# Kernel tuning notes

Hardware: AMD Instinct MI355X
Metric: run time of the kernel (lower is better)

## Reference

```python
import jax, jax.numpy as jnp
import numpy as np

C = 256
A = 3
N = 2
LV = [(160, 240, 4), (80, 120, 8), (40, 60, 16), (20, 30, 32), (10, 15, 64)]  # (H, W, stride)
LVTOP = 1000
IOU_THR = 0.7
POST_TOP = 1000


def _make_priors(h, w, stride):
    ys = (np.arange(h) + 0.5) * stride
    xs = (np.arange(w) + 0.5) * stride
    cy, cx = np.meshgrid(ys, xs, indexing='ij')
    ratios = np.array([0.5, 1.0, 2.0])
    size = stride * 4.0
    ws = size * np.sqrt(ratios)
    hs = size / np.sqrt(ratios)
    x1 = cx[..., None] - ws / 2
    y1 = cy[..., None] - hs / 2
    x2 = cx[..., None] + ws / 2
    y2 = cy[..., None] + hs / 2
    return np.stack([x1, y1, x2, y2], -1).reshape(-1, 4).astype(np.float32)


def setup_inputs() -> dict:
    key = jax.random.key(0)
    ks = jax.random.split(key, 9)
    inp = {}
    for i, (h, w, s) in enumerate(LV):
        inp[f'fmap{i}'] = jax.random.normal(ks[i], (N, C, h, w), jnp.float32)
        inp[f'priors{i}'] = jnp.asarray(_make_priors(h, w, s))
    inp['imsizes'] = jnp.array([[640.0, 960.0]] * N, jnp.float32)  # (h, w) per image
    inp['conv_w'] = jax.random.normal(ks[5], (C, C, 3, 3), jnp.float32) * 0.02
    inp['conv_b'] = jnp.zeros((C,), jnp.float32)
    inp['log_w'] = jax.random.normal(ks[6], (A, C), jnp.float32) * 0.02
    inp['log_b'] = jnp.zeros((A,), jnp.float32)
    inp['reg_w'] = jax.random.normal(ks[7], (A * 4, C), jnp.float32) * 0.02
    inp['reg_b'] = jnp.zeros((A * 4,), jnp.float32)
    return inp


def _forward(fmaps, priors, imsizes, conv_w, conv_b, log_w, log_b, reg_w, reg_b):
    n = fmaps[0].shape[0]
    boxes_l, logit_l, lvidx_l = [], [], []
    for lv, (x, p) in enumerate(zip(fmaps, priors)):
        # 3x3 conv head + relu
        h = jax.lax.conv_general_dilated(x, conv_w, (1, 1), [(1, 1), (1, 1)],
                                         dimension_numbers=('NCHW', 'OIHW', 'NCHW'))
        h = jax.nn.relu(h + conv_b[None, :, None, None])
        # 1x1 heads, permute(0,2,3,1).reshape  -> [n, H*W*A, 4] / [n, H*W*A]
        reg = jnp.einsum('nchw,oc->nhwo', h, reg_w) + reg_b
        log = jnp.einsum('nchw,oc->nhwo', h, log_w) + log_b
        reg = jax.lax.stop_gradient(reg.reshape(n, -1, 4))  # .detach() in torch
        log = jax.lax.stop_gradient(log.reshape(n, -1))
        k = min(LVTOP, log.shape[1])
        val, top = jax.lax.top_k(log, k)                    # per-image level-wise topk
        regt = jnp.take_along_axis(reg, top[..., None], axis=1)  # [n,k,4]
        prit = p[top]                                       # [n,k,4]
        # decode_boxes with mults (1, 1): priors xyxy -> cxcywh, apply deltas
        pw = prit[..., 2] - prit[..., 0]
        ph = prit[..., 3] - prit[..., 1]
        pcx = prit[..., 0] + 0.5 * pw
        pcy = prit[..., 1] + 0.5 * ph
        cx = pcx + regt[..., 0] * pw
        cy = pcy + regt[..., 1] * ph
        bw = pw * jnp.exp(regt[..., 2])
        bh = ph * jnp.exp(regt[..., 3])
        boxes_l.append(jnp.stack([cx - bw / 2, cy - bh / 2, cx + bw / 2, cy + bh / 2], -1))
        logit_l.append(val)
        lvidx_l.append(jnp.full((k,), lv, jnp.int32))
    boxes = jnp.concatenate(boxes_l, 1)                     # [n, K, 4]
    obj = jax.nn.sigmoid(jnp.concatenate(logit_l, 1))       # [n, K]
    lvidx = jnp.concatenate(lvidx_l)                        # [K]
    K = boxes.shape[1]
    # flatten; obj >= 0 keeps everything (sigmoid), min_size=0 removes nothing
    boxes = boxes.reshape(-1, 4)
    obj = obj.reshape(-1)
    imidx = jnp.repeat(jnp.arange(n), K)
    lvidx = jnp.tile(lvidx, n)
    # clamp_to_canvas
    hw = imsizes[imidx]                                     # [M, 2] = (h, w)
    xs = jnp.clip(boxes[:, 0::2], 0.0, hw[:, 1:2])
    ys = jnp.clip(boxes[:, 1::2], 0.0, hw[:, 0:1])
    boxes = jnp.stack([xs[:, 0], ys[:, 0], xs[:, 1], ys[:, 1]], -1)
    # batched_nms via coordinate-offset trick; groups = imidx*10 + level
    groups = (imidx * 10 + lvidx).astype(boxes.dtype)
    off = groups * (jnp.max(boxes) + 1.0)
    bo = boxes + off[:, None]
    order = jnp.argsort(-obj)
    bs = bo[order]
    ss = obj[order]
    ims = imidx[order]
    braw = boxes[order]
    M = bs.shape[0]
    area = (bs[:, 2] - bs[:, 0]) * (bs[:, 3] - bs[:, 1])
    rng = jnp.arange(M)

    def body(i, keep):
        cur = bs[i]
        ix1 = jnp.maximum(cur[0], bs[:, 0])
        iy1 = jnp.maximum(cur[1], bs[:, 1])
        ix2 = jnp.minimum(cur[2], bs[:, 2])
        iy2 = jnp.minimum(cur[3], bs[:, 3])
        inter = jnp.clip(ix2 - ix1, 0.0) * jnp.clip(iy2 - iy1, 0.0)
        iou = inter / jnp.maximum(area[i] + area - inter, 1e-9)
        sup = (iou > IOU_THR) & (rng > i) & keep[i]
        return keep & ~sup

    keep = jax.lax.fori_loop(0, M, body, jnp.ones((M,), bool))
    # per-image top POST_TOP kept boxes, in score order (fixed-shape padded output)
    outs_b, outs_i = [], []
    for i in range(n):
        m = keep & (ims == i)
        sc = jnp.where(m, ss, -jnp.inf)
        v, idx = jax.lax.top_k(sc, POST_TOP)
        valid = v > -jnp.inf
        outs_b.append(jnp.where(valid[:, None], braw[idx], 0.0))
        outs_i.append(jnp.where(valid, i, -1))
    return jnp.stack(outs_b), jnp.stack(outs_i)


def reference(fmap0, fmap1, fmap2, fmap3, fmap4,
              priors0, priors1, priors2, priors3, priors4,
              imsizes, conv_w, conv_b, log_w, log_b, reg_w, reg_b):
    fmaps = [fmap0, fmap1, fmap2, fmap3, fmap4]
    priors = [priors0, priors1, priors2, priors3, priors4]
    return _forward(fmaps, priors, imsizes, conv_w, conv_b, log_w, log_b, reg_w, reg_b)
```

## Files before the change

### kernel.cpp

```cpp
#include <hip/hip_runtime.h>

#define TOTA 153450
#define NGRP 10
#define CK 4
#define CAND_CAP 4096
#define SENT (-3.0e38f)

__device__ __forceinline__ int lv_base(int lv) {
  switch (lv) { case 0: return 0; case 1: return 115200; case 2: return 144000;
                case 3: return 151200; default: return 153000; }
}
__device__ __forceinline__ int lv_of_anchor(int a) {
  if (a < 115200) return 0;
  if (a < 144000) return 1;
  if (a < 151200) return 2;
  if (a < 153000) return 3;
  return 4;
}
__device__ __forceinline__ int kk_of(int lv) { return lv == 4 ? 450 : 1000; }

__device__ __forceinline__ unsigned fkey32(float f) {
  unsigned u = __float_as_uint(f);
  return (u & 0x80000000u) ? ~u : (u | 0x80000000u);
}
__device__ __forceinline__ float inv_fkey32(unsigned k) {
  unsigned u = (k & 0x80000000u) ? (k & 0x7FFFFFFFu) : ~k;
  return __uint_as_float(u);
}

__device__ __forceinline__ float cr_expf(float x) { return (float)exp((double)x); }
__device__ __forceinline__ float cr_sigmoidf(float x) {
  float t = (float)exp(-(double)x);
  float d = 1.0f + t;
  return 1.0f / d;
}

__global__ void transpose_w_kernel(const float* __restrict__ CW, float* __restrict__ WT) {
  int i = blockIdx.x*256 + threadIdx.x;
  if (i >= 2304*256) return;
  int co = i / 2304;
  int k  = i - co*2304;
  WT[(size_t)k*256 + co] = CW[i];
}

#define PPT 2
#define SPT 32
#define XCOLS 34
__global__ __launch_bounds__(256) void conv_head_kernel(
    const float* __restrict__ WT, const float* __restrict__ CB,
    const float* __restrict__ LW, const float* __restrict__ LB,
    const float* __restrict__ RW, const float* __restrict__ RB,
    const float* __restrict__ f0, const float* __restrict__ f1,
    const float* __restrict__ f2, const float* __restrict__ f3,
    const float* __restrict__ f4,
    float* __restrict__ outLog, float* __restrict__ outReg)
{
#pragma clang fp contract(off)
  constexpr int SMEM0 = CK*9*256*4 + 3*CK*XCOLS*4;
  constexpr int SMEM = (SMEM0 > 31744) ? SMEM0 : 31744;
  __shared__ __align__(16) char smem[SMEM];
  float* WS = (float*)smem;
  float* XS = (float*)(smem + CK*9*256*4);
  const int tid = threadIdx.x;
  const int sp = tid & 15;
  const int cg = tid >> 4;

  int bx = blockIdx.x;
  int lv, local;
  if (bx < 1280)      { lv = 0; local = bx; }
  else if (bx < 1600) { lv = 1; local = bx - 1280; }
  else if (bx < 1680) { lv = 2; local = bx - 1600; }
  else if (bx < 1700) { lv = 3; local = bx - 1680; }
  else                { lv = 4; local = bx - 1700; }
  const int TXN[5] = {8, 4, 2, 1, 1};
  const int LH[5]  = {160, 80, 40, 20, 10};
  const int LW_[5] = {240, 120, 60, 30, 15};
  int tx = local % TXN[lv];
  int y  = local / TXN[lv];
  int H = LH[lv], W = LW_[lv];
  int abase = lv_base(lv);
  const float* Xb;
  switch (lv) { case 0: Xb = f0; break; case 1: Xb = f1; break; case 2: Xb = f2; break;
                case 3: Xb = f3; break; default: Xb = f4; }
  const int img = blockIdx.z;
  const float* X = Xb + (size_t)img*256*H*W;
  float* oLog = outLog + (size_t)img*TOTA;
  float* oReg = outReg + (size_t)img*TOTA*4;
  const int x0 = tx * SPT;

  float acc[PPT][16];
  float acc2[PPT][16];
#pragma unroll
  for (int p = 0; p < PPT; ++p)
#pragma unroll
    for (int i = 0; i < 16; ++i) { acc[p][i] = 0.f; acc2[p][i] = 0.f; }

  for (int c0 = 0; c0 < 256; c0 += CK) {
    __syncthreads();
    {
      const float4* wsrc = (const float4*)(WT + (size_t)c0*9*256);
      float4* wdst = (float4*)WS;
#pragma unroll
      for (int r = 0; r < 9; ++r)
        wdst[r*256 + tid] = wsrc[r*256 + tid];
    }
    for (int t = tid; t < 3*CK*XCOLS; t += 256) {
      int col = t % XCOLS; int r = t / XCOLS;
      int ci = r % CK, ry = r / CK;
      int ix = x0 + col - 1, iy = y + ry - 1;
      float v = 0.f;
      if (ix >= 0 && ix < W && iy >= 0 && iy < H)
        v = X[((c0+ci)*H + iy)*W + ix];
      XS[r*XCOLS + col] = v;
    }
    __syncthreads();
#pragma unroll
    for (int ci = 0; ci < CK; ++ci) {
      int ch9 = (c0 + ci) * 9;
#pragma unroll
      for (int k9 = 0; k9 < 9; ++k9) {
        int kglob = ch9 + k9;
        if (kglob == 384 || kglob == 768 || kglob == 1152 ||
            kglob == 1536 || kglob == 1920) {
#pragma unroll
          for (int p = 0; p < PPT; ++p)
#pragma unroll
            for (int i = 0; i < 16; ++i) { acc2[p][i] = acc2[p][i] + acc[p][i]; acc[p][i] = 0.f; }
        }
        int ky = k9 / 3, kx = k9 - ky*3;
        const float* xb = &XS[(ky*CK + ci)*XCOLS + sp + kx];
        float dxv[PPT];
#pragma unroll
        for (int p = 0; p < PPT; ++p) dxv[p] = xb[p*16];
        const float* wr = &WS[(ci*9 + k9)*256 + cg*16];
#pragma unroll
        for (int i = 0; i < 16; i += 4) {
          float4 w4 = *(const float4*)(wr + i);
#pragma unroll
          for (int p = 0; p < PPT; ++p) {
            acc[p][i+0] = fmaf(w4.x, dxv[p], acc[p][i+0]);
            acc[p][i+1] = fmaf(w4.y, dxv[p], acc[p][i+1]);
            acc[p][i+2] = fmaf(w4.z, dxv[p], acc[p][i+2]);
            acc[p][i+3] = fmaf(w4.w, dxv[p], acc[p][i+3]);
          }
        }
      }
    }
  }
  __syncthreads();
  float* HS = (float*)smem;
  float* HWT = (float*)(smem + 16384);
  for (int t = tid; t < 15*256; t += 256) {
    int o = t >> 8, c = t & 255;
    HWT[t] = (o < 3) ? LW[o*256 + c] : RW[(o-3)*256 + c];
  }
#pragma unroll
  for (int px = 0; px < PPT; ++px) {
    __syncthreads();
#pragma unroll
    for (int i = 0; i < 16; ++i) {
      float hsum = acc2[px][i] + acc[px][i];
      float v = hsum + CB[cg*16 + i];
      HS[(cg*16 + i)*16 + sp] = v > 0.f ? v : 0.f;
    }
    __syncthreads();
    if (cg < 15) {
      const float* wr = &HWT[cg*256];
      float a2 = 0.f;
      for (int c = 0; c < 256; ++c) {
        float p = HS[c*16 + sp] * wr[c];
        a2 = a2 + p;
      }
      int gx = x0 + px*16 + sp;
      if (gx < W) {
        int locg = y*W + gx;
        if (cg < 3) {
          oLog[abase + locg*3 + cg] = a2 + LB[cg];
        } else {
          int oo = cg - 3;
          oReg[(size_t)(abase + locg*3 + (oo >> 2))*4 + (oo & 3)] = a2 + RB[oo];
        }
      }
    }
  }
}

__global__ void hist_kernel(const float* __restrict__ logits, unsigned* __restrict__ hist) {
  int i = blockIdx.x*256 + threadIdx.x;
  if (i >= 2*TOTA) return;
  int img = i / TOTA, a = i - img*TOTA;
  int lv = lv_of_anchor(a);
  unsigned k = fkey32(logits[i]);
  atomicAdd(&hist[(size_t)(img*5+lv)*65536 + (k >> 16)], 1u);
}

__global__ __launch_bounds__(256) void thresh_kernel(const unsigned* __restrict__ hist,
                                                     int* __restrict__ meta) {
  int g = blockIdx.x;
  const unsigned* hg = hist + (size_t)g*65536;
  __shared__ unsigned part[256];
  int tid = threadIdx.x;
  unsigned s = 0;
  for (int b = tid*256; b < tid*256 + 256; ++b) s += hg[b];
  part[tid] = s;
  __syncthreads();
  if (tid == 0) {
    int k = kk_of(g % 5);
    unsigned cum = 0; int gsel = 0;
    for (int j = 255; j >= 0; --j) {
      if (cum + part[j] >= (unsigned)k) { gsel = j; break; }
      cum += part[j];
    }
    int B = gsel*256;
    for (int b = gsel*256 + 255; b >= gsel*256; --b) {
      unsigned h = hg[b];
      if (cum + h >= (unsigned)k) { B = b; break; }
      cum += h;
    }
    meta[g] = B;
  }
}

__global__ void collect_kernel(const float* __restrict__ logits, const int* __restrict__ meta,
                               int* __restrict__ ccnt, unsigned long long* __restrict__ cand) {
  int i = blockIdx.x*256 + threadIdx.x;
  if (i >= 2*TOTA) return;
  int img = i / TOTA, a = i - img*TOTA;
  int lv = lv_of_anchor(a);
  int g = img*5 + lv;
  unsigned k = fkey32(logits[i]);
  if ((int)(k >> 16) >= meta[g]) {
    int p = atomicAdd(&ccnt[g], 1);
    if (p < CAND_CAP) {
      unsigned idx = (unsigned)(a - lv_base(lv));
      cand[(size_t)g*CAND_CAP + p] =
          ((unsigned long long)k << 32) | (unsigned long long)(0xFFFFFFFFu ^ idx);
    }
  }
}

__global__ __launch_bounds__(1024) void selsort_kernel(
    const int* __restrict__ ccnt, const unsigned long long* __restrict__ cand,
    float* __restrict__ sellk, unsigned* __restrict__ seli, int* __restrict__ selcnt)
{
  __shared__ unsigned long long KS[CAND_CAP];
  int g = blockIdx.x, tid = threadIdx.x;
  int n = ccnt[g]; if (n > CAND_CAP) n = CAND_CAP;
  for (int t = tid; t < CAND_CAP; t += 1024)
    KS[t] = (t < n) ? cand[(size_t)g*CAND_CAP + t] : 0ULL;
  __syncthreads();
  for (int k2 = 2; k2 <= CAND_CAP; k2 <<= 1)
    for (int j = k2 >> 1; j > 0; j >>= 1) {
      for (int t = tid; t < CAND_CAP/2; t += 1024) {
        int i = (t/j)*(2*j) + (t%j);
        int ix = i + j;
        bool up = ((i & k2) == 0);
        unsigned long long a = KS[i], b = KS[ix];
        if ((a < b) == up) { KS[i] = b; KS[ix] = a; }
      }
      __syncthreads();
    }
  int k = kk_of(g % 5);
  if (tid == 0) selcnt[g] = k;
  for (int t = tid; t < 1024; t += 1024) {
    if (t < k) {
      unsigned long long e = KS[t];
      sellk[(size_t)g*1024 + t] = inv_fkey32((unsigned)(e >> 32));
      seli[(size_t)g*1024 + t] = 0xFFFFFFFFu ^ (unsigned)(e & 0xFFFFFFFFULL);
    } else {
      sellk[(size_t)g*1024 + t] = SENT;
      seli[(size_t)g*1024 + t] = 0u;
    }
  }
}

__global__ __launch_bounds__(1024) void decode_kernel(
    const unsigned* __restrict__ seli, const float* __restrict__ sellk,
    const int* __restrict__ selcnt,
    const float* __restrict__ reg, const float* __restrict__ imsz,
    const float* __restrict__ p0, const float* __restrict__ p1, const float* __restrict__ p2,
    const float* __restrict__ p3, const float* __restrict__ p4,
    float* __restrict__ boxesF, float* __restrict__ selv32)
{
#pragma clang fp contract(off)
  int g = blockIdx.x, t = threadIdx.x;
  int img = g/5, lv = g - img*5;
  int k = selcnt[g];
  float b0 = 0, b1 = 0, b2 = 0, b3 = 0;
  float sv = SENT;
  if (t < k) {
    unsigned aidx = seli[(size_t)g*1024 + t];
    const float* pr;
    switch (lv) { case 0: pr = p0; break; case 1: pr = p1; break; case 2: pr = p2; break;
                  case 3: pr = p3; break; default: pr = p4; }
    pr += (size_t)aidx*4;
    const float* rg = reg + ((size_t)img*TOTA + lv_base(lv) + aidx)*4;
    float q0 = pr[0], q1 = pr[1], q2 = pr[2], q3 = pr[3];
    float pw = q2 - q0, ph = q3 - q1;
    float pcx = q0 + 0.5f*pw, pcy = q1 + 0.5f*ph;
    float t0 = rg[0]*pw, t1 = rg[1]*ph;
    float cx = pcx + t0, cy = pcy + t1;
    float e2 = cr_expf(rg[2]);
    float e3 = cr_expf(rg[3]);
    float bw = pw*e2, bh = ph*e3;
    float x1 = cx - bw*0.5f, y1 = cy - bh*0.5f, x2 = cx + bw*0.5f, y2 = cy + bh*0.5f;
    float mh = imsz[img*2 + 0], mw = imsz[img*2 + 1];
    b0 = fminf(fmaxf(x1, 0.f), mw);
    b1 = fminf(fmaxf(y1, 0.f), mh);
    b2 = fminf(fmaxf(x2, 0.f), mw);
    b3 = fminf(fmaxf(y2, 0.f), mh);
    sv = cr_sigmoidf(sellk[(size_t)g*1024 + t]);
  }
  float* o = boxesF + ((size_t)g*1024 + t)*4;
  o[0] = b0; o[1] = b1; o[2] = b2; o[3] = b3;
  selv32[(size_t)g*1024 + t] = sv;
}

__global__ void maxbox_kernel(const float* __restrict__ boxesF, unsigned* __restrict__ maxbuf) {
  int i = blockIdx.x*1024 + threadIdx.x;
  if (i < NGRP*1024*4) {
    float v = boxesF[i];
    atomicMax(maxbuf, __float_as_uint(v));
  }
}

__global__ __launch_bounds__(256) void mask_kernel(
    const float* __restrict__ boxesF, const int* __restrict__ selcnt,
    const unsigned* __restrict__ maxbuf, unsigned long long* __restrict__ supm)
{
#pragma clang fp contract(off)
  __shared__ float4 BS[1024];
  __shared__ float AR[1024];
  int g = blockIdx.y;
  int i = blockIdx.x*16 + (threadIdx.x >> 4);
  int w = threadIdx.x & 15;
  int img = g/5, lv = g - img*5;
  int k = selcnt[g];
  float mx1 = __uint_as_float(*maxbuf) + 1.0f;
  float offv = (float)(img*10 + lv) * mx1;
  for (int t = threadIdx.x; t < 1024; t += 256) {
    float4 b = ((const float4*)boxesF)[(size_t)g*1024 + t];
    b.x = b.x + offv; b.y = b.y + offv; b.z = b.z + offv; b.w = b.w + offv;
    BS[t] = b;
    float dw = b.z - b.x, dh = b.w - b.y;
    AR[t] = dw*dh;
  }
  __syncthreads();
  unsigned long long m = 0ULL;
  if (i < k) {
    float4 bi = BS[i]; float ai = AR[i];
    int jbase = w*64;
    for (int jj = 0; jj < 64; ++jj) {
      int j = jbase + jj;
      if (j > i && j < k) {
        float4 bj = BS[j];
        float ix1 = fmaxf(bi.x, bj.x), iy1 = fmaxf(bi.y, bj.y);
        float ix2 = fminf(bi.z, bj.z), iy2 = fminf(bi.w, bj.w);
        float d1 = fmaxf(ix2 - ix1, 0.f), d2 = fmaxf(iy2 - iy1, 0.f);
        float inter = d1*d2;
        float un = ai + AR[j];
        un = un - inter;
        float iou = inter / fmaxf(un, 1e-9f);
        if (iou > 0.7f) m |= (1ULL << jj);
      }
    }
  }
  supm[((size_t)g*1024 + i)*16 + w] = m;
}

__global__ __launch_bounds__(64) void nms_scan_kernel(
    const unsigned long long* __restrict__ supm, const int* __restrict__ selcnt,
    unsigned long long* __restrict__ keepw)
{
  __shared__ unsigned long long rem[16];
  int g = blockIdx.x, l = threadIdx.x;
  if (l < 16) rem[l] = 0ULL;
  __syncthreads();
  int k = selcnt[g];
  for (int i = 0; i < k; ++i) {
    bool sup = (rem[i >> 6] >> (i & 63)) & 1ULL;
    __syncthreads();
    if (!sup && l < 16) rem[l] |= supm[((size_t)g*1024 + i)*16 + l];
    __syncthreads();
  }
  if (l < 16) keepw[g*16 + l] = ~rem[l];
}

__global__ __launch_bounds__(1024) void final_kernel(
    const float* __restrict__ selv32, const int* __restrict__ selcnt,
    const unsigned long long* __restrict__ keepw, const float* __restrict__ boxesF,
    float* __restrict__ outB, float* __restrict__ outI)
{
  extern __shared__ unsigned long long S[];
  int img = blockIdx.x, tid = threadIdx.x;
  for (int t = tid; t < 8192; t += 1024) {
    unsigned long long key = 0ULL;
    if (t < 5000) {
      int lv = t / 1000, r = t - lv*1000;
      int g = img*5 + lv;
      if (r < selcnt[g] && ((keepw[g*16 + (r >> 6)] >> (r & 63)) & 1ULL)) {
        float sv = selv32[(size_t)g*1024 + r];
        key = ((unsigned long long)fkey32(sv) << 32) |
              (unsigned long long)(0xFFFFFFFFu ^ (unsigned)t);
      }
    }
    S[t] = key;
  }
  __syncthreads();
  for (int k2 = 2; k2 <= 8192; k2 <<= 1)
    for (int j = k2 >> 1; j > 0; j >>= 1) {
      for (int t = tid; t < 4096; t += 1024) {
        int i = (t/j)*(2*j) + (t%j);
        int ix = i + j;
        bool up = ((i & k2) == 0);
        unsigned long long a = S[i], b = S[ix];
        if ((a < b) == up) { S[i] = b; S[ix] = a; }
      }
      __syncthreads();
    }
  for (int t = tid; t < 1000; t += 1024) {
    unsigned long long key = S[t];
    float4 bo = make_float4(0.f, 0.f, 0.f, 0.f);
    float ii = -1.f;
    if (key != 0ULL) {
      unsigned slot = 0xFFFFFFFFu ^ (unsigned)(key & 0xFFFFFFFFULL);
      int lv = slot / 1000, r = slot - lv*1000;
      const float* bp = boxesF + (((size_t)(img*5 + lv))*1024 + r)*4;
      bo = make_float4(bp[0], bp[1], bp[2], bp[3]);
      ii = (float)img;
    }
    ((float4*)outB)[img*1000 + t] = bo;
    outI[img*1000 + t] = ii;
  }
}

extern "C" void kernel_launch(void* const* d_in, const int* in_sizes, int n_in,
                              void* d_out, int out_size, void* d_ws, size_t ws_size,
                              hipStream_t stream)
{
  const float* fm[5]; const float* pri[5];
  if (n_in >= 17 && in_sizes[1] == 460800) {
    for (int i = 0; i < 5; ++i) { fm[i] = (const float*)d_in[2*i]; pri[i] = (const float*)d_in[2*i+1]; }
  } else {
    for (int i = 0; i < 5; ++i) { fm[i] = (const float*)d_in[i]; pri[i] = (const float*)d_in[5+i]; }
  }
  const float* imsz  = (const float*)d_in[10];
  const float* convw = (const float*)d_in[11];
  const float* convb = (const float*)d_in[12];
  const float* logw  = (const float*)d_in[13];
  const float* logb  = (const float*)d_in[14];
  const float* regw  = (const float*)d_in[15];
  const float* regb  = (const float*)d_in[16];

  char* ws = (char*)d_ws;
  size_t off = 0;
  auto nxt = [&](size_t b) { size_t o = off; off = (off + b + 255) & ~(size_t)255; return o; };
  float* WT        = (float*)(ws + nxt((size_t)2304*256*4));
  float* logitsF   = (float*)(ws + nxt((size_t)2*TOTA*4));
  float* regF      = (float*)(ws + nxt((size_t)2*TOTA*4*4));
  unsigned* hist   = (unsigned*)(ws + nxt((size_t)NGRP*65536*4));
  int* meta        = (int*)(ws + nxt((size_t)NGRP*4));
  int* ccnt        = (int*)(ws + nxt((size_t)NGRP*4));
  unsigned long long* cand = (unsigned long long*)(ws + nxt((size_t)NGRP*CAND_CAP*8));
  float* sellk     = (float*)(ws + nxt((size_t)NGRP*1024*4));
  unsigned* seli   = (unsigned*)(ws + nxt((size_t)NGRP*1024*4));
  int* selcnt      = (int*)(ws + nxt((size_t)NGRP*4));
  float* selv32    = (float*)(ws + nxt((size_t)NGRP*1024*4));
  float* boxesF    = (float*)(ws + nxt((size_t)NGRP*1024*4*4));
  unsigned* maxbuf = (unsigned*)(ws + nxt(4));
  unsigned long long* supm  = (unsigned long long*)(ws + nxt((size_t)NGRP*1024*16*8));
  unsigned long long* keepw = (unsigned long long*)(ws + nxt((size_t)NGRP*16*8));
  if (off > ws_size) return;

  hipMemsetAsync(hist, 0, (size_t)NGRP*65536*4, stream);
  hipMemsetAsync(ccnt, 0, NGRP*4, stream);
  hipMemsetAsync(maxbuf, 0, 4, stream);

  transpose_w_kernel<<<2304, 256, 0, stream>>>(convw, WT);

  {
    dim3 grid(1710, 1, 2);
    conv_head_kernel<<<grid, 256, 0, stream>>>(
        WT, convb, logw, logb, regw, regb,
        fm[0], fm[1], fm[2], fm[3], fm[4],
        logitsF, regF);
  }
  int tot = 2*TOTA;
  hist_kernel<<<(tot + 255)/256, 256, 0, stream>>>(logitsF, hist);
  thresh_kernel<<<NGRP, 256, 0, stream>>>(hist, meta);
  collect_kernel<<<(tot + 255)/256, 256, 0, stream>>>(logitsF, meta, ccnt, cand);
  selsort_kernel<<<NGRP, 1024, 0, stream>>>(ccnt, cand, sellk, seli, selcnt);
  decode_kernel<<<NGRP, 1024, 0, stream>>>(seli, sellk, selcnt, regF, imsz,
      pri[0], pri[1], pri[2], pri[3], pri[4], boxesF, selv32);
  maxbox_kernel<<<(NGRP*1024*4 + 1023)/1024, 1024, 0, stream>>>(boxesF, maxbuf);
  mask_kernel<<<dim3(64, NGRP), 256, 0, stream>>>(boxesF, selcnt, maxbuf, supm);
  nms_scan_kernel<<<NGRP, 64, 0, stream>>>(supm, selcnt, keepw);
  final_kernel<<<2, 1024, 65536, stream>>>(selv32, selcnt, keepw, boxesF,
      (float*)d_out, (float*)d_out + 8000);
}
```

Before: 2.639 ms.

## Register-prefetch next conv channel chunk and use shuffles in NMS scan

```diff
diff --git a/kernel.cpp b/kernel.cpp
--- a/kernel.cpp
+++ b/kernel.cpp
@@ -46,7 +46,8 @@
 #define PPT 2
 #define SPT 32
 #define XCOLS 34
-__global__ __launch_bounds__(256) void conv_head_kernel(
+#define XSN (3*CK*XCOLS)
+__global__ __launch_bounds__(256, 4) void conv_head_kernel(
     const float* __restrict__ WT, const float* __restrict__ CB,
     const float* __restrict__ LW, const float* __restrict__ LB,
     const float* __restrict__ RW, const float* __restrict__ RB,
@@ -56,7 +57,7 @@
     float* __restrict__ outLog, float* __restrict__ outReg)
 {
 #pragma clang fp contract(off)
-  constexpr int SMEM0 = CK*9*256*4 + 3*CK*XCOLS*4;
+  constexpr int SMEM0 = CK*9*256*4 + XSN*4;
   constexpr int SMEM = (SMEM0 > 31744) ? SMEM0 : 31744;
   __shared__ __align__(16) char smem[SMEM];
   float* WS = (float*)smem;
@@ -95,25 +96,41 @@
 #pragma unroll
     for (int i = 0; i < 16; ++i) { acc[p][i] = 0.f; acc2[p][i] = 0.f; }
 
+  float4 wpre[9];
+  float xpre[2];
+  auto prefetch = [&](int c0) {
+    const float4* wsrc = (const float4*)(WT + (size_t)c0*9*256);
+#pragma unroll
+    for (int r = 0; r < 9; ++r) wpre[r] = wsrc[r*256 + tid];
+#pragma unroll
+    for (int u = 0; u < 2; ++u) {
+      int t = tid + u*256;
+      float v = 0.f;
+      if (t < XSN) {
+        int col = t % XCOLS; int r = t / XCOLS;
+        int ci = r % CK, ry = r / CK;
+        int ix = x0 + col - 1, iy = y + ry - 1;
+        if (ix >= 0 && ix < W && iy >= 0 && iy < H)
+          v = X[((size_t)(c0+ci)*H + iy)*W + ix];
+      }
+      xpre[u] = v;
+    }
+  };
+  prefetch(0);
+
   for (int c0 = 0; c0 < 256; c0 += CK) {
+    {
+      float4* wdst = (float4*)WS;
+#pragma unroll
+      for (int r = 0; r < 9; ++r) wdst[r*256 + tid] = wpre[r];
+#pragma unroll
+      for (int u = 0; u < 2; ++u) {
+        int t = tid + u*256;
+        if (t < XSN) XS[t] = xpre[u];
+      }
+    }
     __syncthreads();
-    {
-      const float4* wsrc = (const float4*)(WT + (size_t)c0*9*256);
-      float4* wdst = (float4*)WS;
-#pragma unroll
-      for (int r = 0; r < 9; ++r)
-        wdst[r*256 + tid] = wsrc[r*256 + tid];
-    }
-    for (int t = tid; t < 3*CK*XCOLS; t += 256) {
-      int col = t % XCOLS; int r = t / XCOLS;
-      int ci = r % CK, ry = r / CK;
-      int ix = x0 + col - 1, iy = y + ry - 1;
-      float v = 0.f;
-      if (ix >= 0 && ix < W && iy >= 0 && iy < H)
-        v = X[((c0+ci)*H + iy)*W + ix];
-      XS[r*XCOLS + col] = v;
-    }
-    __syncthreads();
+    if (c0 + CK < 256) prefetch(c0 + CK);
 #pragma unroll
     for (int ci = 0; ci < CK; ++ci) {
       int ch9 = (c0 + ci) * 9;
@@ -146,8 +163,8 @@
         }
       }
     }
-  }
-  __syncthreads();
+    __syncthreads();
+  }
   float* HS = (float*)smem;
   float* HWT = (float*)(smem + 16384);
   for (int t = tid; t < 15*256; t += 256) {
@@ -372,18 +389,15 @@
     const unsigned long long* __restrict__ supm, const int* __restrict__ selcnt,
     unsigned long long* __restrict__ keepw)
 {
-  __shared__ unsigned long long rem[16];
   int g = blockIdx.x, l = threadIdx.x;
-  if (l < 16) rem[l] = 0ULL;
-  __syncthreads();
+  unsigned long long rem = 0ULL;
   int k = selcnt[g];
   for (int i = 0; i < k; ++i) {
-    bool sup = (rem[i >> 6] >> (i & 63)) & 1ULL;
-    __syncthreads();
-    if (!sup && l < 16) rem[l] |= supm[((size_t)g*1024 + i)*16 + l];
-    __syncthreads();
-  }
-  if (l < 16) keepw[g*16 + l] = ~rem[l];
+    unsigned long long wrd = __shfl(rem, i >> 6);
+    bool sup = (wrd >> (i & 63)) & 1ULL;
+    if (!sup && l < 16) rem |= supm[((size_t)g*1024 + i)*16 + l];
+  }
+  if (l < 16) keepw[g*16 + l] = ~rem;
 }
 
 __global__ __launch_bounds__(1024) void final_kernel(
```

Result: slower. 4.660 ms (+76.6%).
